# Optimization experiments

Hardware: AMD Instinct MI355X
Metric: run time of the kernel (lower is better)

## Reference

```python
import jax, jax.numpy as jnp
import numpy as np

N = 20000        # nodes
E = 320000       # edges (avg degree 16)
F_IN = 256       # n_feat
HID = 64         # n_hid (per-head channels, layer 1)
HEADS = 8        # hard-coded n_head in GAT2
NCLS = 64        # n_classes
NEG_SLOPE = 0.2  # PyG GATv2Conv default leaky_relu slope
EPS = 1e-16      # PyG softmax denominator epsilon


def setup_inputs() -> dict:
    key = jax.random.key(0)
    ks = jax.random.split(key, 10)
    glorot = lambda k, shape: jax.random.normal(k, shape, jnp.float32) * (1.0 / np.sqrt(shape[0]))
    return {
        "x": jax.random.normal(ks[0], (N, F_IN), jnp.float32),
        "edge_index": jax.random.randint(ks[1], (2, E), 0, N, dtype=jnp.int32),
        # layer 1: GATv2Conv(F_IN -> HID, heads=HEADS, concat=True)
        "Wl1": glorot(ks[2], (F_IN, HEADS * HID)),
        "Wr1": glorot(ks[3], (F_IN, HEADS * HID)),
        "att1": glorot(ks[4], (HEADS, HID)),
        "b1": jnp.zeros((HEADS * HID,), jnp.float32),
        # layer 2: GATv2Conv(HEADS*HID -> NCLS, heads=1, concat=False)
        "Wl2": glorot(ks[5], (HEADS * HID, NCLS)),
        "Wr2": glorot(ks[6], (HEADS * HID, NCLS)),
        "att2": glorot(ks[7], (1, NCLS)),
        "b2": jnp.zeros((NCLS,), jnp.float32),
    }


def gatv2_layer(x, Wl, Wr, att, bias, src, dst, heads, concat):
    # x: [N, Fin]; Wl/Wr: [Fin, heads*C]; att: [heads, C]
    n = x.shape[0]
    c = att.shape[1]
    xl = (x @ Wl).reshape(n, heads, c)   # source-side projection
    xr = (x @ Wr).reshape(n, heads, c)   # target-side projection
    # per-edge GATv2 score: a^T leaky_relu(Wl x_j + Wr x_i)
    e = jax.nn.leaky_relu(xl[src] + xr[dst], NEG_SLOPE)      # [E, H, C]
    alpha = jnp.einsum('ehc,hc->eh', e, att)                 # [E, H]
    # segment softmax over incoming edges of each target node
    amax = jax.ops.segment_max(alpha, dst, num_segments=n)   # [N, H]
    amax = jnp.where(jnp.isfinite(amax), amax, 0.0)
    ex = jnp.exp(alpha - amax[dst])
    denom = jax.ops.segment_sum(ex, dst, num_segments=n)     # [N, H]
    w = ex / (denom[dst] + EPS)                              # [E, H]
    # weighted scatter-aggregate of source features
    out = jax.ops.segment_sum(xl[src] * w[:, :, None], dst, num_segments=n)  # [N, H, C]
    out = out.reshape(n, heads * c) if concat else out.mean(axis=1)
    return out + bias


def reference(x, edge_index, Wl1, Wr1, att1, b1, Wl2, Wr2, att2, b2):
    src, dst = edge_index[0], edge_index[1]
    h = gatv2_layer(x, Wl1, Wr1, att1, b1, src, dst, HEADS, True)   # [N, 512]
    h = jax.nn.elu(h)
    out = gatv2_layer(h, Wl2, Wr2, att2, b2, src, dst, 1, False)    # [N, 64]
    return out
```

## Files before the change

### kernel.cpp

```cpp
#include <hip/hip_runtime.h>
#include <hip/hip_bf16.h>

#define N_NODES 20000
#define N_EDGES 320000
#define F_IN 256
#define HID 64
#define HEADS 8
#define NCLS 64
#define D1 (HEADS * HID)
#define SCAN_BLOCKS ((N_NODES + 255) / 256)

typedef __attribute__((ext_vector_type(8))) short short8;
typedef __attribute__((ext_vector_type(4))) float floatx4;
typedef __attribute__((ext_vector_type(2))) float v2f;

__device__ __forceinline__ ushort f2bf(float f) {
    unsigned u = __float_as_uint(f);
    unsigned r = (u + 0x7fffu + ((u >> 16) & 1u)) >> 16;
    return (ushort)r;
}
__device__ __forceinline__ float bf2f(ushort u) {
    return __uint_as_float((unsigned)u << 16);
}
__device__ __forceinline__ v2f unpack2(unsigned u) {
    v2f r;
    r.x = __uint_as_float(u << 16);
    r.y = __uint_as_float(u & 0xffff0000u);
    return r;
}
template <int CTRL>
__device__ __forceinline__ float dppadd(float x) {
    int y = __builtin_amdgcn_update_dpp(0, __float_as_int(x), CTRL, 0xF, 0xF, true);
    return x + __int_as_float(y);
}
__device__ __forceinline__ float rowsum16(float x) {
    x = dppadd<0xB1>(x);
    x = dppadd<0x4E>(x);
    x = dppadd<0x124>(x);
    x = dppadd<0x128>(x);
    return x;
}
__device__ __forceinline__ float rowsum32(float x) {
    x = rowsum16(x);
    float t = __int_as_float(__builtin_amdgcn_ds_swizzle(__float_as_int(x), 0x401F));
    return x + t;
}

#define PB_HIST 1250
#define PB_CONV 5000
#define PB_T1   512
#define PB_T2   128
#define PB_TOTAL (PB_HIST + PB_CONV + 2 * PB_T1 + 2 * PB_T2)
__global__ __launch_bounds__(256) void preprocess(
    const float* __restrict__ x, ushort* __restrict__ xbf,
    const float* __restrict__ Wl1, const float* __restrict__ Wr1,
    const float* __restrict__ Wl2, const float* __restrict__ Wr2,
    ushort* __restrict__ wt1, ushort* __restrict__ wt2,
    const int* __restrict__ dst, int* __restrict__ cnt) {
    int b = blockIdx.x, t = threadIdx.x;
    if (b < PB_HIST) {
        int i = b * 256 + t;
        if (i < N_EDGES) atomicAdd(&cnt[dst[i]], 1);
    } else if (b < PB_HIST + PB_CONV) {
        int i = (b - PB_HIST) * 256 + t;
        if (i < N_NODES * F_IN / 4) {
            float4 v = ((const float4*)x)[i];
            ushort4 o;
            o.x = f2bf(v.x); o.y = f2bf(v.y); o.z = f2bf(v.z); o.w = f2bf(v.w);
            ((ushort4*)xbf)[i] = o;
        }
    } else if (b < PB_HIST + PB_CONV + 2 * PB_T1) {
        int lb = b - PB_HIST - PB_CONV;
        const float* W = (lb < PB_T1) ? Wl1 : Wr1;
        ushort* Wt = wt1 + ((lb < PB_T1) ? 0 : D1 * F_IN);
        int i = (lb % PB_T1) * 256 + t;
        if (i < D1 * F_IN) {
            int n = i >> 8, k = i & 255;
            Wt[i] = f2bf(W[(size_t)k * D1 + n]);
        }
    } else {
        int lb = b - PB_HIST - PB_CONV - 2 * PB_T1;
        const float* W = (lb < PB_T2) ? Wl2 : Wr2;
        ushort* Wt = wt2 + ((lb < PB_T2) ? 0 : NCLS * D1);
        int i = (lb % PB_T2) * 256 + t;
        if (i < NCLS * D1) {
            int n = i >> 9, k = i & 511;
            Wt[i] = f2bf(W[(size_t)k * NCLS + n]);
        }
    }
}

__global__ __launch_bounds__(256) void scan_local(const int* __restrict__ cnt,
                                                  int* __restrict__ pscan,
                                                  int* __restrict__ bsum, int n) {
    int tid = threadIdx.x;
    int i = blockIdx.x * 256 + tid;
    int lane = tid & 63, wave = tid >> 6;
    int v = (i < n) ? cnt[i] : 0;
    int x = v;
    #pragma unroll
    for (int d = 1; d < 64; d <<= 1) {
        int y = __shfl_up(x, d);
        if (lane >= d) x += y;
    }
    __shared__ int wsum[4];
    if (lane == 63) wsum[wave] = x;
    __syncthreads();
    int woff = 0;
    for (int w2 = 0; w2 < wave; w2++) woff += wsum[w2];
    int incl = x + woff;
    if (i < n) pscan[i] = incl;
    if (tid == 255) bsum[blockIdx.x] = incl;
}

__global__ __launch_bounds__(128) void scan_block(int* __restrict__ bsum, int nb) {
    int tid = threadIdx.x;
    __shared__ int sh[128];
    int v = (tid < nb) ? bsum[tid] : 0;
    sh[tid] = v;
    __syncthreads();
    #pragma unroll
    for (int d = 1; d < 128; d <<= 1) {
        int x = (tid >= d) ? sh[tid - d] : 0;
        __syncthreads();
        sh[tid] += x;
        __syncthreads();
    }
    if (tid < nb) bsum[tid] = sh[tid] - v;
}

__global__ __launch_bounds__(256) void scan_finalize(const int* __restrict__ cnt,
                                                     const int* __restrict__ pscan,
                                                     const int* __restrict__ bsum,
                                                     int* __restrict__ row_ptr,
                                                     int* __restrict__ cursor, int n) {
    int i = blockIdx.x * 256 + threadIdx.x;
    if (i < n) {
        int incl = pscan[i] + bsum[blockIdx.x];
        row_ptr[i + 1] = incl;
        cursor[i] = incl - cnt[i];
    }
    if (i == 0) row_ptr[0] = 0;
}

__global__ void scatter_kernel(const int* __restrict__ src, const int* __restrict__ dst,
                               int* __restrict__ cursor, int* __restrict__ csr_src, int E) {
    int i = blockIdx.x * 256 + threadIdx.x;
    if (i < E) {
        int d = dst[i];
        int pos = atomicAdd(&cursor[d], 1);
        csr_src[pos] = src[i];
    }
}

#define APAD 40
__global__ __launch_bounds__(256) void gemm_mfma_bt_bf16(
    const ushort* __restrict__ A, const ushort* __restrict__ Bt,
    ushort* __restrict__ C, int M, int N, int K) {
    __shared__ ushort As[128 * APAD];
    __shared__ ushort Bs[64 * APAD];
    int tid = threadIdx.x;
    int rowBase = blockIdx.y * 128, colBase = blockIdx.x * 64;
    int wave = tid >> 6, lane = tid & 63;
    int quad = lane >> 4, m16 = lane & 15;
    floatx4 acc[2][4];
    #pragma unroll
    for (int i = 0; i < 2; i++)
        #pragma unroll
        for (int j = 0; j < 4; j++) acc[i][j] = (floatx4){0.f, 0.f, 0.f, 0.f};

    for (int k0 = 0; k0 < K; k0 += 32) {
        #pragma unroll
        for (int i = 0; i < 2; i++) {
            int idx = i * 256 + tid;
            int r = idx >> 2, kq = (idx & 3) * 8;
            int grow = rowBase + r;
            uint4 v = make_uint4(0, 0, 0, 0);
            if (grow < M) v = *(const uint4*)(A + (size_t)grow * K + k0 + kq);
            *(uint4*)&As[r * APAD + kq] = v;
        }
        {
            int r = tid >> 2, kq = (tid & 3) * 8;
            uint4 v = *(const uint4*)(Bt + (size_t)(colBase + r) * K + k0 + kq);
            *(uint4*)&Bs[r * APAD + kq] = v;
        }
        __syncthreads();
        short8 a0 = *(short8*)&As[(wave * 32 + m16) * APAD + quad * 8];
        short8 a1 = *(short8*)&As[(wave * 32 + 16 + m16) * APAD + quad * 8];
        #pragma unroll
        for (int ct = 0; ct < 4; ct++) {
            short8 b = *(short8*)&Bs[(ct * 16 + m16) * APAD + quad * 8];
            acc[0][ct] = __builtin_amdgcn_mfma_f32_16x16x32_bf16(a0, b, acc[0][ct], 0, 0, 0);
            acc[1][ct] = __builtin_amdgcn_mfma_f32_16x16x32_bf16(a1, b, acc[1][ct], 0, 0, 0);
        }
        __syncthreads();
    }
    #pragma unroll
    for (int rt = 0; rt < 2; rt++)
        #pragma unroll
        for (int ct = 0; ct < 4; ct++)
            #pragma unroll
            for (int r = 0; r < 4; r++) {
                int row = rowBase + wave * 32 + rt * 16 + quad * 4 + r;
                if (row < M) C[(size_t)row * N + colBase + ct * 16 + m16] = f2bf(acc[rt][ct][r]);
            }
}

__global__ __launch_bounds__(128) void attn_l1_fused(
    const ushort* __restrict__ xlr, const float* __restrict__ att,
    const float* __restrict__ b1,
    const int* __restrict__ row_ptr, const int* __restrict__ csr_src,
    ushort* __restrict__ h1out) {
    int d = blockIdx.x, t = threadIdx.x;
    int start = row_ptr[d], deg = row_ptr[d + 1] - start;

    uint2 xru = *(const uint2*)(xlr + (size_t)d * 1024 + 512 + 4 * t);
    v2f xr01 = unpack2(xru.x), xr23 = unpack2(xru.y);
    float4 atv = *(const float4*)(att + 4 * t);
    v2f at6_01 = {0.6f * atv.x, 0.6f * atv.y}, at6_23 = {0.6f * atv.z, 0.6f * atv.w};
    v2f at4_01 = {0.4f * atv.x, 0.4f * atv.y}, at4_23 = {0.4f * atv.z, 0.4f * atv.w};

    float den = 0.f;
    v2f acc01 = {0.f, 0.f}, acc23 = {0.f, 0.f};

    if (deg > 0) {
        uint2 xv[4];
        #pragma unroll
        for (int j = 0; j < 4; j++) {
            int s = csr_src[start + min(j, deg - 1)];
            xv[j] = *(const uint2*)(xlr + (size_t)s * 1024 + 4 * t);
        }
        for (int p0 = 0; p0 < deg; p0 += 4) {
            uint2 u0 = xv[0], u1 = xv[1], u2 = xv[2], u3 = xv[3];
            #pragma unroll
            for (int j = 0; j < 4; j++) {
                int p = p0 + 4 + j;
                if (p < deg) {
                    int s = csr_src[start + p];
                    xv[j] = *(const uint2*)(xlr + (size_t)s * 1024 + 4 * t);
                }
            }
            v2f c01_0 = unpack2(u0.x), c23_0 = unpack2(u0.y);
            v2f c01_1 = unpack2(u1.x), c23_1 = unpack2(u1.y);
            v2f c01_2 = unpack2(u2.x), c23_2 = unpack2(u2.y);
            v2f c01_3 = unpack2(u3.x), c23_3 = unpack2(u3.y);

            v2f va, vb, sp;
            va = c01_0 + xr01; vb = c23_0 + xr23;
            sp = at6_01 * va + at4_01 * __builtin_elementwise_abs(va)
               + at6_23 * vb + at4_23 * __builtin_elementwise_abs(vb);
            float s0 = sp.x + sp.y;
            va = c01_1 + xr01; vb = c23_1 + xr23;
            sp = at6_01 * va + at4_01 * __builtin_elementwise_abs(va)
               + at6_23 * vb + at4_23 * __builtin_elementwise_abs(vb);
            float s1 = sp.x + sp.y;
            va = c01_2 + xr01; vb = c23_2 + xr23;
            sp = at6_01 * va + at4_01 * __builtin_elementwise_abs(va)
               + at6_23 * vb + at4_23 * __builtin_elementwise_abs(vb);
            float s2 = sp.x + sp.y;
            va = c01_3 + xr01; vb = c23_3 + xr23;
            sp = at6_01 * va + at4_01 * __builtin_elementwise_abs(va)
               + at6_23 * vb + at4_23 * __builtin_elementwise_abs(vb);
            float s3 = sp.x + sp.y;

            s0 = rowsum16(s0); s1 = rowsum16(s1);
            s2 = rowsum16(s2); s3 = rowsum16(s3);

            float e0 = (p0 + 0 < deg) ? __expf(s0) : 0.f;
            float e1 = (p0 + 1 < deg) ? __expf(s1) : 0.f;
            float e2 = (p0 + 2 < deg) ? __expf(s2) : 0.f;
            float e3 = (p0 + 3 < deg) ? __expf(s3) : 0.f;
            den += (e0 + e1) + (e2 + e3);
            v2f e0v = {e0, e0}, e1v = {e1, e1}, e2v = {e2, e2}, e3v = {e3, e3};
            acc01 = acc01 + e0v * c01_0 + e1v * c01_1 + e2v * c01_2 + e3v * c01_3;
            acc23 = acc23 + e0v * c23_0 + e1v * c23_1 + e2v * c23_2 + e3v * c23_3;
        }
    }
    float inv = 1.f / (den + 1e-16f);
    float4 bv = *(const float4*)(b1 + 4 * t);
    float o0 = acc01.x * inv + bv.x;
    float o1 = acc01.y * inv + bv.y;
    float o2 = acc23.x * inv + bv.z;
    float o3 = acc23.y * inv + bv.w;
    o0 = o0 > 0.f ? o0 : (__expf(o0) - 1.f);
    o1 = o1 > 0.f ? o1 : (__expf(o1) - 1.f);
    o2 = o2 > 0.f ? o2 : (__expf(o2) - 1.f);
    o3 = o3 > 0.f ? o3 : (__expf(o3) - 1.f);
    ushort4 hv;
    hv.x = f2bf(o0); hv.y = f2bf(o1); hv.z = f2bf(o2); hv.w = f2bf(o3);
    *(ushort4*)(h1out + (size_t)d * D1 + 4 * t) = hv;
}

__global__ __launch_bounds__(256) void attn_l2_fused(
    const ushort* __restrict__ ylr, const float* __restrict__ att2,
    const float* __restrict__ b2,
    const int* __restrict__ row_ptr, const int* __restrict__ csr_src,
    float* __restrict__ out) {
    int wave = threadIdx.x >> 6, lane = threadIdx.x & 63;
    int d = blockIdx.x * 4 + wave;
    if (d >= N_NODES) return;
    int half = lane >> 5, l31 = lane & 31;
    int start = row_ptr[d], deg = row_ptr[d + 1] - start;

    unsigned yru = *(const unsigned*)(ylr + (size_t)d * 128 + 64 + 2 * l31);
    v2f yr2 = unpack2(yru);
    float2 a2 = *(const float2*)(att2 + 2 * l31);
    v2f at6 = {0.6f * a2.x, 0.6f * a2.y};
    v2f at4 = {0.4f * a2.x, 0.4f * a2.y};

    float den = 0.f;
    v2f acc = {0.f, 0.f};

    if (deg > 0) {
        int S = (deg + 1) >> 1;
        unsigned yv[4];
        #pragma unroll
        for (int j = 0; j < 4; j++) {
            int p = min(2 * j + half, deg - 1);
            int s = csr_src[start + p];
            yv[j] = *(const unsigned*)(ylr + (size_t)s * 128 + 2 * l31);
        }
        for (int i = 0; i < S; i++) {
            unsigned cu = yv[i & 3];
            int pf = i + 4;
            if (pf < S) {
                int p = min(2 * pf + half, deg - 1);
                int s = csr_src[start + p];
                yv[i & 3] = *(const unsigned*)(ylr + (size_t)s * 128 + 2 * l31);
            }
            v2f c2 = unpack2(cu);
            v2f v = c2 + yr2;
            v2f sp = at6 * v + at4 * __builtin_elementwise_abs(v);
            float sc = sp.x + sp.y;
            sc = rowsum32(sc);
            float e = (2 * i + half < deg) ? __expf(sc) : 0.f;
            den += e;
            v2f ev = {e, e};
            acc = acc + ev * c2;
        }
        den += __shfl_xor(den, 32);
        acc.x += __shfl_xor(acc.x, 32);
        acc.y += __shfl_xor(acc.y, 32);
    }
    if (half == 0) {
        float inv = 1.f / (den + 1e-16f);
        float2 bv = *(const float2*)(b2 + 2 * l31);
        float2 o;
        o.x = acc.x * inv + bv.x;
        o.y = acc.y * inv + bv.y;
        *(float2*)(out + (size_t)d * NCLS + 2 * l31) = o;
    }
}

extern "C" void kernel_launch(void* const* d_in, const int* in_sizes, int n_in,
                              void* d_out, int out_size, void* d_ws, size_t ws_size,
                              hipStream_t stream) {
    const float* x    = (const float*)d_in[0];
    const int*   edge = (const int*)d_in[1];
    const float* Wl1  = (const float*)d_in[2];
    const float* Wr1  = (const float*)d_in[3];
    const float* att1 = (const float*)d_in[4];
    const float* b1   = (const float*)d_in[5];
    const float* Wl2  = (const float*)d_in[6];
    const float* Wr2  = (const float*)d_in[7];
    const float* att2 = (const float*)d_in[8];
    const float* b2   = (const float*)d_in[9];
    float* out = (float*)d_out;

    const int* srcv = edge;
    const int* dstv = edge + N_EDGES;

    ushort* xbf  = (ushort*)d_ws;
    ushort* wt1  = xbf + (size_t)N_NODES * F_IN;
    ushort* wt2  = wt1 + 2 * D1 * F_IN;
    ushort* xlr  = wt2 + 2 * NCLS * D1;
    ushort* h1   = xlr + (size_t)N_NODES * 2 * D1;
    ushort* ylr  = h1 + (size_t)N_NODES * D1;
    int* cnt     = (int*)(ylr + (size_t)N_NODES * 2 * NCLS);
    int* pscan   = cnt + N_NODES;
    int* bsum    = pscan + N_NODES;
    int* row_ptr = bsum + 128;
    int* cursor  = row_ptr + N_NODES + 1;
    int* csr_src = cursor + N_NODES;

    hipMemsetAsync(cnt, 0, N_NODES * sizeof(int), stream);
    preprocess<<<PB_TOTAL, 256, 0, stream>>>(x, xbf, Wl1, Wr1, Wl2, Wr2, wt1, wt2, dstv, cnt);
    scan_local<<<SCAN_BLOCKS, 256, 0, stream>>>(cnt, pscan, bsum, N_NODES);
    scan_block<<<1, 128, 0, stream>>>(bsum, SCAN_BLOCKS);
    scan_finalize<<<SCAN_BLOCKS, 256, 0, stream>>>(cnt, pscan, bsum, row_ptr, cursor, N_NODES);
    scatter_kernel<<<N_EDGES / 256, 256, 0, stream>>>(srcv, dstv, cursor, csr_src, N_EDGES);

    gemm_mfma_bt_bf16<<<dim3(2 * D1 / 64, (N_NODES + 127) / 128), 256, 0, stream>>>(
        xbf, wt1, xlr, N_NODES, 2 * D1, F_IN);
    attn_l1_fused<<<N_NODES, 128, 0, stream>>>(xlr, att1, b1, row_ptr, csr_src, h1);
    gemm_mfma_bt_bf16<<<dim3(2 * NCLS / 64, (N_NODES + 127) / 128), 256, 0, stream>>>(
        h1, wt2, ylr, N_NODES, 2 * NCLS, D1);
    attn_l2_fused<<<(N_NODES + 3) / 4, 256, 0, stream>>>(ylr, att2, b2, row_ptr, csr_src, out);
}
```

Baseline: 238.6 us.

## Fold block-scan into finalize, use 128x128 GEMM tile, double-buffer L1 gathers

The separate single-block scan kernel is removed. Each finalize block now reduces the preceding block sums itself with wave shuffles, which saves one kernel launch. The layer-1 projection GEMM switches to a new 128x128 tile kernel with 4x4 MFMA accumulators per wave, giving more operand reuse per LDS load but higher register pressure. The layer-1 attention loop gains a second 4-edge prefetch buffer so eight neighbor rows are in flight, which hides gather latency at the cost of more registers.

```diff
diff --git a/kernel.cpp b/kernel.cpp
--- a/kernel.cpp
+++ b/kernel.cpp
@@ -113,30 +113,25 @@
     if (tid == 255) bsum[blockIdx.x] = incl;
 }
 
-__global__ __launch_bounds__(128) void scan_block(int* __restrict__ bsum, int nb) {
-    int tid = threadIdx.x;
-    __shared__ int sh[128];
-    int v = (tid < nb) ? bsum[tid] : 0;
-    sh[tid] = v;
-    __syncthreads();
-    #pragma unroll
-    for (int d = 1; d < 128; d <<= 1) {
-        int x = (tid >= d) ? sh[tid - d] : 0;
-        __syncthreads();
-        sh[tid] += x;
-        __syncthreads();
-    }
-    if (tid < nb) bsum[tid] = sh[tid] - v;
-}
-
 __global__ __launch_bounds__(256) void scan_finalize(const int* __restrict__ cnt,
                                                      const int* __restrict__ pscan,
                                                      const int* __restrict__ bsum,
                                                      int* __restrict__ row_ptr,
                                                      int* __restrict__ cursor, int n) {
-    int i = blockIdx.x * 256 + threadIdx.x;
+    int t = threadIdx.x;
+    int lane = t & 63, wave = t >> 6;
+    int v = (t < SCAN_BLOCKS && t < blockIdx.x) ? bsum[t] : 0;
+    #pragma unroll
+    for (int mask = 1; mask < 64; mask <<= 1) v += __shfl_xor(v, mask);
+    __shared__ int ws[4];
+    __shared__ int soff;
+    if (lane == 0) ws[wave] = v;
+    __syncthreads();
+    if (t == 0) soff = ws[0] + ws[1] + ws[2] + ws[3];
+    __syncthreads();
+    int i = blockIdx.x * 256 + t;
     if (i < n) {
-        int incl = pscan[i] + bsum[blockIdx.x];
+        int incl = pscan[i] + soff;
         row_ptr[i + 1] = incl;
         cursor[i] = incl - cnt[i];
     }
@@ -154,6 +149,60 @@
 }
 
 #define APAD 40
+__global__ __launch_bounds__(256) void gemm_mfma_128x128(
+    const ushort* __restrict__ A, const ushort* __restrict__ Bt,
+    ushort* __restrict__ C, int M, int N, int K) {
+    __shared__ ushort As[128 * APAD];
+    __shared__ ushort Bs[128 * APAD];
+    int tid = threadIdx.x;
+    int rowBase = blockIdx.y * 128, colBase = blockIdx.x * 128;
+    int wave = tid >> 6, lane = tid & 63;
+    int quad = lane >> 4, m16 = lane & 15;
+    int rh = wave >> 1, chf = wave & 1;
+    floatx4 acc[4][4];
+    #pragma unroll
+    for (int i = 0; i < 4; i++)
+        #pragma unroll
+        for (int j = 0; j < 4; j++) acc[i][j] = (floatx4){0.f, 0.f, 0.f, 0.f};
+
+    for (int k0 = 0; k0 < K; k0 += 32) {
+        #pragma unroll
+        for (int i = 0; i < 2; i++) {
+            int idx = i * 256 + tid;
+            int r = idx >> 2, kq = (idx & 3) * 8;
+            int grow = rowBase + r;
+            uint4 v = make_uint4(0, 0, 0, 0);
+            if (grow < M) v = *(const uint4*)(A + (size_t)grow * K + k0 + kq);
+            *(uint4*)&As[r * APAD + kq] = v;
+            uint4 w = *(const uint4*)(Bt + (size_t)(colBase + r) * K + k0 + kq);
+            *(uint4*)&Bs[r * APAD + kq] = w;
+        }
+        __syncthreads();
+        short8 af[4], bf[4];
+        #pragma unroll
+        for (int i = 0; i < 4; i++)
+            af[i] = *(short8*)&As[(rh * 64 + i * 16 + m16) * APAD + quad * 8];
+        #pragma unroll
+        for (int j = 0; j < 4; j++)
+            bf[j] = *(short8*)&Bs[(chf * 64 + j * 16 + m16) * APAD + quad * 8];
+        #pragma unroll
+        for (int i = 0; i < 4; i++)
+            #pragma unroll
+            for (int j = 0; j < 4; j++)
+                acc[i][j] = __builtin_amdgcn_mfma_f32_16x16x32_bf16(af[i], bf[j], acc[i][j], 0, 0, 0);
+        __syncthreads();
+    }
+    #pragma unroll
+    for (int i = 0; i < 4; i++)
+        #pragma unroll
+        for (int j = 0; j < 4; j++)
+            #pragma unroll
+            for (int r = 0; r < 4; r++) {
+                int row = rowBase + rh * 64 + i * 16 + quad * 4 + r;
+                if (row < M) C[(size_t)row * N + colBase + chf * 64 + j * 16 + m16] = f2bf(acc[i][j][r]);
+            }
+}
+
 __global__ __launch_bounds__(256) void gemm_mfma_bt_bf16(
     const ushort* __restrict__ A, const ushort* __restrict__ Bt,
     ushort* __restrict__ C, int M, int N, int K) {
@@ -224,56 +273,102 @@
     v2f acc01 = {0.f, 0.f}, acc23 = {0.f, 0.f};
 
     if (deg > 0) {
-        uint2 xv[4];
+        uint2 bufA[4], bufB[4];
         #pragma unroll
         for (int j = 0; j < 4; j++) {
             int s = csr_src[start + min(j, deg - 1)];
-            xv[j] = *(const uint2*)(xlr + (size_t)s * 1024 + 4 * t);
-        }
-        for (int p0 = 0; p0 < deg; p0 += 4) {
-            uint2 u0 = xv[0], u1 = xv[1], u2 = xv[2], u3 = xv[3];
-            #pragma unroll
-            for (int j = 0; j < 4; j++) {
-                int p = p0 + 4 + j;
-                if (p < deg) {
-                    int s = csr_src[start + p];
-                    xv[j] = *(const uint2*)(xlr + (size_t)s * 1024 + 4 * t);
+            bufA[j] = *(const uint2*)(xlr + (size_t)s * 1024 + 4 * t);
+        }
+        #pragma unroll
+        for (int j = 0; j < 4; j++) {
+            int s = csr_src[start + min(4 + j, deg - 1)];
+            bufB[j] = *(const uint2*)(xlr + (size_t)s * 1024 + 4 * t);
+        }
+        for (int p0 = 0; p0 < deg; p0 += 8) {
+            {
+                uint2 u0 = bufA[0], u1 = bufA[1], u2 = bufA[2], u3 = bufA[3];
+                #pragma unroll
+                for (int j = 0; j < 4; j++) {
+                    int p = p0 + 8 + j;
+                    if (p < deg) {
+                        int s = csr_src[start + p];
+                        bufA[j] = *(const uint2*)(xlr + (size_t)s * 1024 + 4 * t);
+                    }
                 }
+                v2f c01_0 = unpack2(u0.x), c23_0 = unpack2(u0.y);
+                v2f c01_1 = unpack2(u1.x), c23_1 = unpack2(u1.y);
+                v2f c01_2 = unpack2(u2.x), c23_2 = unpack2(u2.y);
+                v2f c01_3 = unpack2(u3.x), c23_3 = unpack2(u3.y);
+                v2f va, vb, sp;
+                va = c01_0 + xr01; vb = c23_0 + xr23;
+                sp = at6_01 * va + at4_01 * __builtin_elementwise_abs(va)
+                   + at6_23 * vb + at4_23 * __builtin_elementwise_abs(vb);
+                float s0 = sp.x + sp.y;
+                va = c01_1 + xr01; vb = c23_1 + xr23;
+                sp = at6_01 * va + at4_01 * __builtin_elementwise_abs(va)
+                   + at6_23 * vb + at4_23 * __builtin_elementwise_abs(vb);
+                float s1 = sp.x + sp.y;
+                va = c01_2 + xr01; vb = c23_2 + xr23;
+                sp = at6_01 * va + at4_01 * __builtin_elementwise_abs(va)
+                   + at6_23 * vb + at4_23 * __builtin_elementwise_abs(vb);
+                float s2 = sp.x + sp.y;
+                va = c01_3 + xr01; vb = c23_3 + xr23;
+                sp = at6_01 * va + at4_01 * __builtin_elementwise_abs(va)
+                   + at6_23 * vb + at4_23 * __builtin_elementwise_abs(vb);
+                float s3 = sp.x + sp.y;
+                s0 = rowsum16(s0); s1 = rowsum16(s1);
+                s2 = rowsum16(s2); s3 = rowsum16(s3);
+                float e0 = (p0 + 0 < deg) ? __expf(s0) : 0.f;
+                float e1 = (p0 + 1 < deg) ? __expf(s1) : 0.f;
+                float e2 = (p0 + 2 < deg) ? __expf(s2) : 0.f;
+                float e3 = (p0 + 3 < deg) ? __expf(s3) : 0.f;
+                den += (e0 + e1) + (e2 + e3);
+                v2f e0v = {e0, e0}, e1v = {e1, e1}, e2v = {e2, e2}, e3v = {e3, e3};
+                acc01 = acc01 + e0v * c01_0 + e1v * c01_1 + e2v * c01_2 + e3v * c01_3;
+                acc23 = acc23 + e0v * c23_0 + e1v * c23_1 + e2v * c23_2 + e3v * c23_3;
             }
-            v2f c01_0 = unpack2(u0.x), c23_0 = unpack2(u0.y);
-            v2f c01_1 = unpack2(u1.x), c23_1 = unpack2(u1.y);
-            v2f c01_2 = unpack2(u2.x), c23_2 = unpack2(u2.y);
-            v2f c01_3 = unpack2(u3.x), c23_3 = unpack2(u3.y);
-
-            v2f va, vb, sp;
-            va = c01_0 + xr01; vb = c23_0 + xr23;
-            sp = at6_01 * va + at4_01 * __builtin_elementwise_abs(va)
-               + at6_23 * vb + at4_23 * __builtin_elementwise_abs(vb);
-            float s0 = sp.x + sp.y;
-            va = c01_1 + xr01; vb = c23_1 + xr23;
-            sp = at6_01 * va + at4_01 * __builtin_elementwise_abs(va)
-               + at6_23 * vb + at4_23 * __builtin_elementwise_abs(vb);
-            float s1 = sp.x + sp.y;
-            va = c01_2 + xr01; vb = c23_2 + xr23;
-            sp = at6_01 * va + at4_01 * __builtin_elementwise_abs(va)
-               + at6_23 * vb + at4_23 * __builtin_elementwise_abs(vb);
-            float s2 = sp.x + sp.y;
-            va = c01_3 + xr01; vb = c23_3 + xr23;
-            sp = at6_01 * va + at4_01 * __builtin_elementwise_abs(va)
-               + at6_23 * vb + at4_23 * __builtin_elementwise_abs(vb);
-            float s3 = sp.x + sp.y;
-
-            s0 = rowsum16(s0); s1 = rowsum16(s1);
-            s2 = rowsum16(s2); s3 = rowsum16(s3);
-
-            float e0 = (p0 + 0 < deg) ? __expf(s0) : 0.f;
-            float e1 = (p0 + 1 < deg) ? __expf(s1) : 0.f;
-            float e2 = (p0 + 2 < deg) ? __expf(s2) : 0.f;
-            float e3 = (p0 + 3 < deg) ? __expf(s3) : 0.f;
-            den += (e0 + e1) + (e2 + e3);
-            v2f e0v = {e0, e0}, e1v = {e1, e1}, e2v = {e2, e2}, e3v = {e3, e3};
-            acc01 = acc01 + e0v * c01_0 + e1v * c01_1 + e2v * c01_2 + e3v * c01_3;
-            acc23 = acc23 + e0v * c23_0 + e1v * c23_1 + e2v * c23_2 + e3v * c23_3;
+            if (p0 + 4 < deg) {
+                uint2 u0 = bufB[0], u1 = bufB[1], u2 = bufB[2], u3 = bufB[3];
+                #pragma unroll
+                for (int j = 0; j < 4; j++) {
+                    int p = p0 + 12 + j;
+                    if (p < deg) {
+                        int s = csr_src[start + p];
+                        bufB[j] = *(const uint2*)(xlr + (size_t)s * 1024 + 4 * t);
+                    }
+                }
+                v2f c01_0 = unpack2(u0.x), c23_0 = unpack2(u0.y);
+                v2f c01_1 = unpack2(u1.x), c23_1 = unpack2(u1.y);
+                v2f c01_2 = unpack2(u2.x), c23_2 = unpack2(u2.y);
+                v2f c01_3 = unpack2(u3.x), c23_3 = unpack2(u3.y);
+                v2f va, vb, sp;
+                va = c01_0 + xr01; vb = c23_0 + xr23;
+                sp = at6_01 * va + at4_01 * __builtin_elementwise_abs(va)
+                   + at6_23 * vb + at4_23 * __builtin_elementwise_abs(vb);
+                float s0 = sp.x + sp.y;
+                va = c01_1 + xr01; vb = c23_1 + xr23;
+                sp = at6_01 * va + at4_01 * __builtin_elementwise_abs(va)
+                   + at6_23 * vb + at4_23 * __builtin_elementwise_abs(vb);
+                float s1 = sp.x + sp.y;
+                va = c01_2 + xr01; vb = c23_2 + xr23;
+                sp = at6_01 * va + at4_01 * __builtin_elementwise_abs(va)
+                   + at6_23 * vb + at4_23 * __builtin_elementwise_abs(vb);
+                float s2 = sp.x + sp.y;
+                va = c01_3 + xr01; vb = c23_3 + xr23;
+                sp = at6_01 * va + at4_01 * __builtin_elementwise_abs(va)
+                   + at6_23 * vb + at4_23 * __builtin_elementwise_abs(vb);
+                float s3 = sp.x + sp.y;
+                s0 = rowsum16(s0); s1 = rowsum16(s1);
+                s2 = rowsum16(s2); s3 = rowsum16(s3);
+                float e0 = (p0 + 4 < deg) ? __expf(s0) : 0.f;
+                float e1 = (p0 + 5 < deg) ? __expf(s1) : 0.f;
+                float e2 = (p0 + 6 < deg) ? __expf(s2) : 0.f;
+                float e3 = (p0 + 7 < deg) ? __expf(s3) : 0.f;
+                den += (e0 + e1) + (e2 + e3);
+                v2f e0v = {e0, e0}, e1v = {e1, e1}, e2v = {e2, e2}, e3v = {e3, e3};
+                acc01 = acc01 + e0v * c01_0 + e1v * c01_1 + e2v * c01_2 + e3v * c01_3;
+                acc23 = acc23 + e0v * c23_0 + e1v * c23_1 + e2v * c23_2 + e3v * c23_3;
+            }
         }
     }
     float inv = 1.f / (den + 1e-16f);
@@ -386,11 +481,10 @@
     hipMemsetAsync(cnt, 0, N_NODES * sizeof(int), stream);
     preprocess<<<PB_TOTAL, 256, 0, stream>>>(x, xbf, Wl1, Wr1, Wl2, Wr2, wt1, wt2, dstv, cnt);
     scan_local<<<SCAN_BLOCKS, 256, 0, stream>>>(cnt, pscan, bsum, N_NODES);
-    scan_block<<<1, 128, 0, stream>>>(bsum, SCAN_BLOCKS);
     scan_finalize<<<SCAN_BLOCKS, 256, 0, stream>>>(cnt, pscan, bsum, row_ptr, cursor, N_NODES);
     scatter_kernel<<<N_EDGES / 256, 256, 0, stream>>>(srcv, dstv, cursor, csr_src, N_EDGES);
 
-    gemm_mfma_bt_bf16<<<dim3(2 * D1 / 64, (N_NODES + 127) / 128), 256, 0, stream>>>(
+    gemm_mfma_128x128<<<dim3(2 * D1 / 128, (N_NODES + 127) / 128), 256, 0, stream>>>(
         xbf, wt1, xlr, N_NODES, 2 * D1, F_IN);
     attn_l1_fused<<<N_NODES, 128, 0, stream>>>(xlr, att1, b1, row_ptr, csr_src, h1);
     gemm_mfma_bt_bf16<<<dim3(2 * NCLS / 64, (N_NODES + 127) / 128), 256, 0, stream>>>(
```

Result: no change. 236.5 us (-0.9%).

## Merge scan into one kernel, fuse scatter with GEMM1, retile GEMMs, restructure attention

Applied to the files above, without the earlier changes.

Replaces the three-kernel prefix scan with a single 1024-thread block scan and launches the CSR scatter as extra blocks of the first GEMM, which cuts the launch count. GEMM1 moves to 128x128 tiles and GEMM2 gets a dedicated 32x128 kernel. Layer-1 attention now assigns one wave per half of the edges, with each lane holding 8 channels, and merges the two waves through shared memory. Both attention layers fold log2(e) into the attention weights so they can call exp2f. The trade-offs are a serial single-block scan and more register pressure in the larger GEMM tile.

```diff
diff --git a/kernel.cpp b/kernel.cpp
--- a/kernel.cpp
+++ b/kernel.cpp
@@ -8,7 +8,6 @@
 #define HEADS 8
 #define NCLS 64
 #define D1 (HEADS * HID)
-#define SCAN_BLOCKS ((N_NODES + 255) / 256)
 
 typedef __attribute__((ext_vector_type(8))) short short8;
 typedef __attribute__((ext_vector_type(4))) float floatx4;
@@ -18,9 +17,6 @@
     unsigned u = __float_as_uint(f);
     unsigned r = (u + 0x7fffu + ((u >> 16) & 1u)) >> 16;
     return (ushort)r;
-}
-__device__ __forceinline__ float bf2f(ushort u) {
-    return __uint_as_float((unsigned)u << 16);
 }
 __device__ __forceinline__ v2f unpack2(unsigned u) {
     v2f r;
@@ -32,6 +28,12 @@
 __device__ __forceinline__ float dppadd(float x) {
     int y = __builtin_amdgcn_update_dpp(0, __float_as_int(x), CTRL, 0xF, 0xF, true);
     return x + __int_as_float(y);
+}
+__device__ __forceinline__ float rowsum8(float x) {
+    x = dppadd<0xB1>(x);
+    x = dppadd<0x4E>(x);
+    x = dppadd<0x141>(x);
+    return x;
 }
 __device__ __forceinline__ float rowsum16(float x) {
     x = dppadd<0xB1>(x);
@@ -90,82 +92,69 @@
     }
 }
 
-__global__ __launch_bounds__(256) void scan_local(const int* __restrict__ cnt,
-                                                  int* __restrict__ pscan,
-                                                  int* __restrict__ bsum, int n) {
+__global__ __launch_bounds__(1024) void scan_all(const int* __restrict__ cnt,
+                                                 int* __restrict__ row_ptr,
+                                                 int* __restrict__ cursor) {
+    __shared__ int wsum[16];
+    __shared__ int s_running;
+    int t = threadIdx.x, lane = t & 63, wv = t >> 6;
+    if (t == 0) { s_running = 0; row_ptr[0] = 0; }
+    __syncthreads();
+    for (int base = 0; base < N_NODES; base += 1024) {
+        int i = base + t;
+        int v = (i < N_NODES) ? cnt[i] : 0;
+        int x = v;
+        #pragma unroll
+        for (int d = 1; d < 64; d <<= 1) {
+            int y = __shfl_up(x, d);
+            if (lane >= d) x += y;
+        }
+        if (lane == 63) wsum[wv] = x;
+        __syncthreads();
+        int woff = 0;
+        for (int k = 0; k < wv; k++) woff += wsum[k];
+        int run = s_running;
+        int incl = x + woff + run;
+        if (i < N_NODES) {
+            row_ptr[i + 1] = incl;
+            cursor[i] = incl - v;
+        }
+        __syncthreads();
+        if (t == 1023) s_running = incl;
+        __syncthreads();
+    }
+}
+
+#define APAD 40
+#define G1_NT 8
+#define G1_MT ((N_NODES + 127) / 128)
+#define G1_BLOCKS (G1_NT * G1_MT)
+#define SC_BLOCKS (N_EDGES / 256)
+__global__ __launch_bounds__(256) void gemm1_scatter(
+    const ushort* __restrict__ A, const ushort* __restrict__ Bt,
+    ushort* __restrict__ C,
+    const int* __restrict__ src, const int* __restrict__ dst,
+    int* __restrict__ cursor, int* __restrict__ csr_src) {
+    if (blockIdx.x >= G1_BLOCKS) {
+        int i = (blockIdx.x - G1_BLOCKS) * 256 + threadIdx.x;
+        if (i < N_EDGES) {
+            int d = dst[i];
+            int pos = atomicAdd(&cursor[d], 1);
+            csr_src[pos] = src[i];
+        }
+        return;
+    }
+    const int M = N_NODES, N = 2 * D1, K = F_IN;
+    __shared__ ushort As[128 * APAD];
+    __shared__ ushort Bs[128 * APAD];
     int tid = threadIdx.x;
-    int i = blockIdx.x * 256 + tid;
-    int lane = tid & 63, wave = tid >> 6;
-    int v = (i < n) ? cnt[i] : 0;
-    int x = v;
-    #pragma unroll
-    for (int d = 1; d < 64; d <<= 1) {
-        int y = __shfl_up(x, d);
-        if (lane >= d) x += y;
-    }
-    __shared__ int wsum[4];
-    if (lane == 63) wsum[wave] = x;
-    __syncthreads();
-    int woff = 0;
-    for (int w2 = 0; w2 < wave; w2++) woff += wsum[w2];
-    int incl = x + woff;
-    if (i < n) pscan[i] = incl;
-    if (tid == 255) bsum[blockIdx.x] = incl;
-}
-
-__global__ __launch_bounds__(128) void scan_block(int* __restrict__ bsum, int nb) {
-    int tid = threadIdx.x;
-    __shared__ int sh[128];
-    int v = (tid < nb) ? bsum[tid] : 0;
-    sh[tid] = v;
-    __syncthreads();
-    #pragma unroll
-    for (int d = 1; d < 128; d <<= 1) {
-        int x = (tid >= d) ? sh[tid - d] : 0;
-        __syncthreads();
-        sh[tid] += x;
-        __syncthreads();
-    }
-    if (tid < nb) bsum[tid] = sh[tid] - v;
-}
-
-__global__ __launch_bounds__(256) void scan_finalize(const int* __restrict__ cnt,
-                                                     const int* __restrict__ pscan,
-                                                     const int* __restrict__ bsum,
-                                                     int* __restrict__ row_ptr,
-                                                     int* __restrict__ cursor, int n) {
-    int i = blockIdx.x * 256 + threadIdx.x;
-    if (i < n) {
-        int incl = pscan[i] + bsum[blockIdx.x];
-        row_ptr[i + 1] = incl;
-        cursor[i] = incl - cnt[i];
-    }
-    if (i == 0) row_ptr[0] = 0;
-}
-
-__global__ void scatter_kernel(const int* __restrict__ src, const int* __restrict__ dst,
-                               int* __restrict__ cursor, int* __restrict__ csr_src, int E) {
-    int i = blockIdx.x * 256 + threadIdx.x;
-    if (i < E) {
-        int d = dst[i];
-        int pos = atomicAdd(&cursor[d], 1);
-        csr_src[pos] = src[i];
-    }
-}
-
-#define APAD 40
-__global__ __launch_bounds__(256) void gemm_mfma_bt_bf16(
-    const ushort* __restrict__ A, const ushort* __restrict__ Bt,
-    ushort* __restrict__ C, int M, int N, int K) {
-    __shared__ ushort As[128 * APAD];
-    __shared__ ushort Bs[64 * APAD];
-    int tid = threadIdx.x;
-    int rowBase = blockIdx.y * 128, colBase = blockIdx.x * 64;
+    int rowBase = (blockIdx.x >> 3) * 128, colBase = (blockIdx.x & 7) * 128;
     int wave = tid >> 6, lane = tid & 63;
     int quad = lane >> 4, m16 = lane & 15;
-    floatx4 acc[2][4];
+    int rh = wave >> 1, chf = wave & 1;
+    floatx4 acc[4][4];
     #pragma unroll
-    for (int i = 0; i < 2; i++)
+    for (int i = 0; i < 4; i++)
         #pragma unroll
         for (int j = 0; j < 4; j++) acc[i][j] = (floatx4){0.f, 0.f, 0.f, 0.f};
 
@@ -178,31 +167,87 @@
             uint4 v = make_uint4(0, 0, 0, 0);
             if (grow < M) v = *(const uint4*)(A + (size_t)grow * K + k0 + kq);
             *(uint4*)&As[r * APAD + kq] = v;
-        }
-        {
-            int r = tid >> 2, kq = (tid & 3) * 8;
-            uint4 v = *(const uint4*)(Bt + (size_t)(colBase + r) * K + k0 + kq);
-            *(uint4*)&Bs[r * APAD + kq] = v;
-        }
-        __syncthreads();
-        short8 a0 = *(short8*)&As[(wave * 32 + m16) * APAD + quad * 8];
-        short8 a1 = *(short8*)&As[(wave * 32 + 16 + m16) * APAD + quad * 8];
-        #pragma unroll
-        for (int ct = 0; ct < 4; ct++) {
-            short8 b = *(short8*)&Bs[(ct * 16 + m16) * APAD + quad * 8];
-            acc[0][ct] = __builtin_amdgcn_mfma_f32_16x16x32_bf16(a0, b, acc[0][ct], 0, 0, 0);
-            acc[1][ct] = __builtin_amdgcn_mfma_f32_16x16x32_bf16(a1, b, acc[1][ct], 0, 0, 0);
-        }
+            uint4 w = *(const uint4*)(Bt + (size_t)(colBase + r) * K + k0 + kq);
+            *(uint4*)&Bs[r * APAD + kq] = w;
+        }
+        __syncthreads();
+        short8 af[4], bfr[4];
+        #pragma unroll
+        for (int i = 0; i < 4; i++)
+            af[i] = *(short8*)&As[(rh * 64 + i * 16 + m16) * APAD + quad * 8];
+        #pragma unroll
+        for (int j = 0; j < 4; j++)
+            bfr[j] = *(short8*)&Bs[(chf * 64 + j * 16 + m16) * APAD + quad * 8];
+        #pragma unroll
+        for (int i = 0; i < 4; i++)
+            #pragma unroll
+            for (int j = 0; j < 4; j++)
+                acc[i][j] = __builtin_amdgcn_mfma_f32_16x16x32_bf16(af[i], bfr[j], acc[i][j], 0, 0, 0);
         __syncthreads();
     }
     #pragma unroll
-    for (int rt = 0; rt < 2; rt++)
-        #pragma unroll
-        for (int ct = 0; ct < 4; ct++)
+    for (int i = 0; i < 4; i++)
+        #pragma unroll
+        for (int j = 0; j < 4; j++)
             #pragma unroll
             for (int r = 0; r < 4; r++) {
-                int row = rowBase + wave * 32 + rt * 16 + quad * 4 + r;
-                if (row < M) C[(size_t)row * N + colBase + ct * 16 + m16] = f2bf(acc[rt][ct][r]);
+                int row = rowBase + rh * 64 + i * 16 + quad * 4 + r;
+                if (row < M) C[(size_t)row * N + colBase + chf * 64 + j * 16 + m16] = f2bf(acc[i][j][r]);
+            }
+}
+
+__global__ __launch_bounds__(256) void gemm2_32x128(
+    const ushort* __restrict__ A, const ushort* __restrict__ Bt,
+    ushort* __restrict__ C) {
+    const int K = D1;
+    __shared__ ushort As[32 * APAD];
+    __shared__ ushort Bs[128 * APAD];
+    int tid = threadIdx.x;
+    int rowBase = blockIdx.x * 32;
+    int wave = tid >> 6, lane = tid & 63;
+    int quad = lane >> 4, m16 = lane & 15;
+    floatx4 acc[2][2];
+    #pragma unroll
+    for (int i = 0; i < 2; i++)
+        #pragma unroll
+        for (int j = 0; j < 2; j++) acc[i][j] = (floatx4){0.f, 0.f, 0.f, 0.f};
+
+    for (int k0 = 0; k0 < K; k0 += 32) {
+        if (tid < 128) {
+            int r = tid >> 2, kq = (tid & 3) * 8;
+            uint4 v = *(const uint4*)(A + (size_t)(rowBase + r) * K + k0 + kq);
+            *(uint4*)&As[r * APAD + kq] = v;
+        }
+        #pragma unroll
+        for (int i = 0; i < 2; i++) {
+            int idx = i * 256 + tid;
+            int r = idx >> 2, kq = (idx & 3) * 8;
+            uint4 v = *(const uint4*)(Bt + (size_t)r * K + k0 + kq);
+            *(uint4*)&Bs[r * APAD + kq] = v;
+        }
+        __syncthreads();
+        short8 af[2], bfr[2];
+        #pragma unroll
+        for (int i = 0; i < 2; i++)
+            af[i] = *(short8*)&As[(i * 16 + m16) * APAD + quad * 8];
+        #pragma unroll
+        for (int j = 0; j < 2; j++)
+            bfr[j] = *(short8*)&Bs[(wave * 32 + j * 16 + m16) * APAD + quad * 8];
+        #pragma unroll
+        for (int i = 0; i < 2; i++)
+            #pragma unroll
+            for (int j = 0; j < 2; j++)
+                acc[i][j] = __builtin_amdgcn_mfma_f32_16x16x32_bf16(af[i], bfr[j], acc[i][j], 0, 0, 0);
+        __syncthreads();
+    }
+    #pragma unroll
+    for (int i = 0; i < 2; i++)
+        #pragma unroll
+        for (int j = 0; j < 2; j++)
+            #pragma unroll
+            for (int r = 0; r < 4; r++) {
+                int row = rowBase + i * 16 + quad * 4 + r;
+                C[(size_t)row * 128 + wave * 32 + j * 16 + m16] = f2bf(acc[i][j][r]);
             }
 }
 
@@ -211,84 +256,93 @@
     const float* __restrict__ b1,
     const int* __restrict__ row_ptr, const int* __restrict__ csr_src,
     ushort* __restrict__ h1out) {
-    int d = blockIdx.x, t = threadIdx.x;
+    int d = blockIdx.x;
+    int wave = threadIdx.x >> 6, lane = threadIdx.x & 63;
     int start = row_ptr[d], deg = row_ptr[d + 1] - start;
 
-    uint2 xru = *(const uint2*)(xlr + (size_t)d * 1024 + 512 + 4 * t);
+    uint4 xru = *(const uint4*)(xlr + (size_t)d * 1024 + 512 + 8 * lane);
     v2f xr01 = unpack2(xru.x), xr23 = unpack2(xru.y);
-    float4 atv = *(const float4*)(att + 4 * t);
-    v2f at6_01 = {0.6f * atv.x, 0.6f * atv.y}, at6_23 = {0.6f * atv.z, 0.6f * atv.w};
-    v2f at4_01 = {0.4f * atv.x, 0.4f * atv.y}, at4_23 = {0.4f * atv.z, 0.4f * atv.w};
+    v2f xr45 = unpack2(xru.z), xr67 = unpack2(xru.w);
+    const float C6 = 0.6f * 1.44269504f, C4 = 0.4f * 1.44269504f;
+    float4 atA = *(const float4*)(att + 8 * lane);
+    float4 atB = *(const float4*)(att + 8 * lane + 4);
+    v2f a6_01 = {C6 * atA.x, C6 * atA.y}, a4_01 = {C4 * atA.x, C4 * atA.y};
+    v2f a6_23 = {C6 * atA.z, C6 * atA.w}, a4_23 = {C4 * atA.z, C4 * atA.w};
+    v2f a6_45 = {C6 * atB.x, C6 * atB.y}, a4_45 = {C4 * atB.x, C4 * atB.y};
+    v2f a6_67 = {C6 * atB.z, C6 * atB.w}, a4_67 = {C4 * atB.z, C4 * atB.w};
 
     float den = 0.f;
-    v2f acc01 = {0.f, 0.f}, acc23 = {0.f, 0.f};
-
-    if (deg > 0) {
-        uint2 xv[4];
+    v2f ac01 = {0.f, 0.f}, ac23 = {0.f, 0.f}, ac45 = {0.f, 0.f}, ac67 = {0.f, 0.f};
+
+    int S = (deg > wave) ? ((deg - wave + 1) >> 1) : 0;
+    if (S > 0) {
+        uint4 buf[4];
         #pragma unroll
         for (int j = 0; j < 4; j++) {
-            int s = csr_src[start + min(j, deg - 1)];
-            xv[j] = *(const uint2*)(xlr + (size_t)s * 1024 + 4 * t);
-        }
-        for (int p0 = 0; p0 < deg; p0 += 4) {
-            uint2 u0 = xv[0], u1 = xv[1], u2 = xv[2], u3 = xv[3];
-            #pragma unroll
-            for (int j = 0; j < 4; j++) {
-                int p = p0 + 4 + j;
-                if (p < deg) {
-                    int s = csr_src[start + p];
-                    xv[j] = *(const uint2*)(xlr + (size_t)s * 1024 + 4 * t);
-                }
+            int s = csr_src[start + wave + 2 * min(j, S - 1)];
+            buf[j] = *(const uint4*)(xlr + (size_t)s * 1024 + 8 * lane);
+        }
+        for (int i = 0; i < S; i++) {
+            uint4 cu = buf[i & 3];
+            int ip = i + 4;
+            if (ip < S) {
+                int s = csr_src[start + wave + 2 * ip];
+                buf[i & 3] = *(const uint4*)(xlr + (size_t)s * 1024 + 8 * lane);
             }
-            v2f c01_0 = unpack2(u0.x), c23_0 = unpack2(u0.y);
-            v2f c01_1 = unpack2(u1.x), c23_1 = unpack2(u1.y);
-            v2f c01_2 = unpack2(u2.x), c23_2 = unpack2(u2.y);
-            v2f c01_3 = unpack2(u3.x), c23_3 = unpack2(u3.y);
-
-            v2f va, vb, sp;
-            va = c01_0 + xr01; vb = c23_0 + xr23;
-            sp = at6_01 * va + at4_01 * __builtin_elementwise_abs(va)
-               + at6_23 * vb + at4_23 * __builtin_elementwise_abs(vb);
-            float s0 = sp.x + sp.y;
-            va = c01_1 + xr01; vb = c23_1 + xr23;
-            sp = at6_01 * va + at4_01 * __builtin_elementwise_abs(va)
-               + at6_23 * vb + at4_23 * __builtin_elementwise_abs(vb);
-            float s1 = sp.x + sp.y;
-            va = c01_2 + xr01; vb = c23_2 + xr23;
-            sp = at6_01 * va + at4_01 * __builtin_elementwise_abs(va)
-               + at6_23 * vb + at4_23 * __builtin_elementwise_abs(vb);
-            float s2 = sp.x + sp.y;
-            va = c01_3 + xr01; vb = c23_3 + xr23;
-            sp = at6_01 * va + at4_01 * __builtin_elementwise_abs(va)
-               + at6_23 * vb + at4_23 * __builtin_elementwise_abs(vb);
-            float s3 = sp.x + sp.y;
-
-            s0 = rowsum16(s0); s1 = rowsum16(s1);
-            s2 = rowsum16(s2); s3 = rowsum16(s3);
-
-            float e0 = (p0 + 0 < deg) ? __expf(s0) : 0.f;
-            float e1 = (p0 + 1 < deg) ? __expf(s1) : 0.f;
-            float e2 = (p0 + 2 < deg) ? __expf(s2) : 0.f;
-            float e3 = (p0 + 3 < deg) ? __expf(s3) : 0.f;
-            den += (e0 + e1) + (e2 + e3);
-            v2f e0v = {e0, e0}, e1v = {e1, e1}, e2v = {e2, e2}, e3v = {e3, e3};
-            acc01 = acc01 + e0v * c01_0 + e1v * c01_1 + e2v * c01_2 + e3v * c01_3;
-            acc23 = acc23 + e0v * c23_0 + e1v * c23_1 + e2v * c23_2 + e3v * c23_3;
-        }
-    }
-    float inv = 1.f / (den + 1e-16f);
-    float4 bv = *(const float4*)(b1 + 4 * t);
-    float o0 = acc01.x * inv + bv.x;
-    float o1 = acc01.y * inv + bv.y;
-    float o2 = acc23.x * inv + bv.z;
-    float o3 = acc23.y * inv + bv.w;
-    o0 = o0 > 0.f ? o0 : (__expf(o0) - 1.f);
-    o1 = o1 > 0.f ? o1 : (__expf(o1) - 1.f);
-    o2 = o2 > 0.f ? o2 : (__expf(o2) - 1.f);
-    o3 = o3 > 0.f ? o3 : (__expf(o3) - 1.f);
-    ushort4 hv;
-    hv.x = f2bf(o0); hv.y = f2bf(o1); hv.z = f2bf(o2); hv.w = f2bf(o3);
-    *(ushort4*)(h1out + (size_t)d * D1 + 4 * t) = hv;
+            v2f c01 = unpack2(cu.x), c23 = unpack2(cu.y);
+            v2f c45 = unpack2(cu.z), c67 = unpack2(cu.w);
+            v2f v01 = c01 + xr01, v23 = c23 + xr23;
+            v2f v45 = c45 + xr45, v67 = c67 + xr67;
+            v2f sp = a6_01 * v01 + a4_01 * __builtin_elementwise_abs(v01);
+            sp = sp + a6_23 * v23 + a4_23 * __builtin_elementwise_abs(v23);
+            sp = sp + a6_45 * v45 + a4_45 * __builtin_elementwise_abs(v45);
+            sp = sp + a6_67 * v67 + a4_67 * __builtin_elementwise_abs(v67);
+            float sc = sp.x + sp.y;
+            sc = rowsum8(sc);
+            float e = exp2f(sc);
+            den += e;
+            v2f ev = {e, e};
+            ac01 = ac01 + ev * c01; ac23 = ac23 + ev * c23;
+            ac45 = ac45 + ev * c45; ac67 = ac67 + ev * c67;
+        }
+    }
+    __shared__ float sden[128];
+    __shared__ float sacc[2][64][8];
+    sden[wave * 64 + lane] = den;
+    float4 f0 = {ac01.x, ac01.y, ac23.x, ac23.y};
+    float4 f1 = {ac45.x, ac45.y, ac67.x, ac67.y};
+    *(float4*)&sacc[wave][lane][0] = f0;
+    *(float4*)&sacc[wave][lane][4] = f1;
+    __syncthreads();
+    if (wave == 0) {
+        den += sden[64 + lane];
+        float4 g0 = *(float4*)&sacc[1][lane][0];
+        float4 g1 = *(float4*)&sacc[1][lane][4];
+        float inv = 1.f / (den + 1e-16f);
+        float4 bA = *(const float4*)(b1 + 8 * lane);
+        float4 bB = *(const float4*)(b1 + 8 * lane + 4);
+        float o0 = (ac01.x + g0.x) * inv + bA.x;
+        float o1 = (ac01.y + g0.y) * inv + bA.y;
+        float o2 = (ac23.x + g0.z) * inv + bA.z;
+        float o3 = (ac23.y + g0.w) * inv + bA.w;
+        float o4 = (ac45.x + g1.x) * inv + bB.x;
+        float o5 = (ac45.y + g1.y) * inv + bB.y;
+        float o6 = (ac67.x + g1.z) * inv + bB.z;
+        float o7 = (ac67.y + g1.w) * inv + bB.w;
+        o0 = o0 > 0.f ? o0 : (__expf(o0) - 1.f);
+        o1 = o1 > 0.f ? o1 : (__expf(o1) - 1.f);
+        o2 = o2 > 0.f ? o2 : (__expf(o2) - 1.f);
+        o3 = o3 > 0.f ? o3 : (__expf(o3) - 1.f);
+        o4 = o4 > 0.f ? o4 : (__expf(o4) - 1.f);
+        o5 = o5 > 0.f ? o5 : (__expf(o5) - 1.f);
+        o6 = o6 > 0.f ? o6 : (__expf(o6) - 1.f);
+        o7 = o7 > 0.f ? o7 : (__expf(o7) - 1.f);
+        ushort4 h0, h1v;
+        h0.x = f2bf(o0); h0.y = f2bf(o1); h0.z = f2bf(o2); h0.w = f2bf(o3);
+        h1v.x = f2bf(o4); h1v.y = f2bf(o5); h1v.z = f2bf(o6); h1v.w = f2bf(o7);
+        *(ushort4*)(h1out + (size_t)d * D1 + 8 * lane) = h0;
+        *(ushort4*)(h1out + (size_t)d * D1 + 8 * lane + 4) = h1v;
+    }
 }
 
 __global__ __launch_bounds__(256) void attn_l2_fused(
@@ -305,8 +359,9 @@
     unsigned yru = *(const unsigned*)(ylr + (size_t)d * 128 + 64 + 2 * l31);
     v2f yr2 = unpack2(yru);
     float2 a2 = *(const float2*)(att2 + 2 * l31);
-    v2f at6 = {0.6f * a2.x, 0.6f * a2.y};
-    v2f at4 = {0.4f * a2.x, 0.4f * a2.y};
+    const float C6 = 0.6f * 1.44269504f, C4 = 0.4f * 1.44269504f;
+    v2f at6 = {C6 * a2.x, C6 * a2.y};
+    v2f at4 = {C4 * a2.x, C4 * a2.y};
 
     float den = 0.f;
     v2f acc = {0.f, 0.f};
@@ -333,7 +388,7 @@
             v2f sp = at6 * v + at4 * __builtin_elementwise_abs(v);
             float sc = sp.x + sp.y;
             sc = rowsum32(sc);
-            float e = (2 * i + half < deg) ? __expf(sc) : 0.f;
+            float e = (2 * i + half < deg) ? exp2f(sc) : 0.f;
             den += e;
             v2f ev = {e, e};
             acc = acc + ev * c2;
@@ -377,23 +432,16 @@
     ushort* h1   = xlr + (size_t)N_NODES * 2 * D1;
     ushort* ylr  = h1 + (size_t)N_NODES * D1;
     int* cnt     = (int*)(ylr + (size_t)N_NODES * 2 * NCLS);
-    int* pscan   = cnt + N_NODES;
-    int* bsum    = pscan + N_NODES;
-    int* row_ptr = bsum + 128;
+    int* row_ptr = cnt + N_NODES;
     int* cursor  = row_ptr + N_NODES + 1;
     int* csr_src = cursor + N_NODES;
 
     hipMemsetAsync(cnt, 0, N_NODES * sizeof(int), stream);
     preprocess<<<PB_TOTAL, 256, 0, stream>>>(x, xbf, Wl1, Wr1, Wl2, Wr2, wt1, wt2, dstv, cnt);
-    scan_local<<<SCAN_BLOCKS, 256, 0, stream>>>(cnt, pscan, bsum, N_NODES);
-    scan_block<<<1, 128, 0, stream>>>(bsum, SCAN_BLOCKS);
-    scan_finalize<<<SCAN_BLOCKS, 256, 0, stream>>>(cnt, pscan, bsum, row_ptr, cursor, N_NODES);
-    scatter_kernel<<<N_EDGES / 256, 256, 0, stream>>>(srcv, dstv, cursor, csr_src, N_EDGES);
-
-    gemm_mfma_bt_bf16<<<dim3(2 * D1 / 64, (N_NODES + 127) / 128), 256, 0, stream>>>(
-        xbf, wt1, xlr, N_NODES, 2 * D1, F_IN);
+    scan_all<<<1, 1024, 0, stream>>>(cnt, row_ptr, cursor);
+    gemm1_scatter<<<G1_BLOCKS + SC_BLOCKS, 256, 0, stream>>>(
+        xbf, wt1, xlr, srcv, dstv, cursor, csr_src);
     attn_l1_fused<<<N_NODES, 128, 0, stream>>>(xlr, att1, b1, row_ptr, csr_src, h1);
-    gemm_mfma_bt_bf16<<<dim3(2 * NCLS / 64, (N_NODES + 127) / 128), 256, 0, stream>>>(
-        h1, wt2, ylr, N_NODES, 2 * NCLS, D1);
+    gemm2_32x128<<<N_NODES / 32, 256, 0, stream>>>(h1, wt2, ylr);
     attn_l2_fused<<<(N_NODES + 3) / 4, 256, 0, stream>>>(ylr, att2, b2, row_ptr, csr_src, out);
 }
```

Result: slower. 332.8 us (+39.5%).
